# Performance work log

Measured on AMD Instinct MI355X. Metric: run time of the kernel, lower is better.

Reference implementation:

```python
import jax, jax.numpy as jnp
import numpy as np
import math


def closest_square_factors(N):
    s = int(math.isqrt(N))
    for i in range(s, 0, -1):
        if N % i == 0:
            return (i, N // i)


def landmark_pool(t, num_landmarks):
    # t: [B, H, N, Dh]; CLS token kept, rest avg-pooled on a 2D grid to num_landmarks.
    B, H, N, Dh = t.shape
    w1, w2 = closest_square_factors(N - 1)   # token grid (32, 32)
    h, w = closest_square_factors(num_landmarks)  # landmark grid (8, 8)
    assert w1 % h == 0 and w2 % w == 0  # divisible -> adaptive pool == uniform pool
    cls = t[:, :, :1, :]
    rest = t[:, :, 1:, :].reshape(B, H, h, w1 // h, w, w2 // w, Dh)
    pooled = rest.mean(axis=(3, 5)).reshape(B, H, num_landmarks, Dh)
    return jnp.concatenate([cls, pooled], axis=2)  # [B, H, num_landmarks+1, Dh]


def moore_penrose_iter_pinv(x, iters=6):
    # x: [..., m, m]; iterative Newton-Schulz style pseudo-inverse.
    abs_x = jnp.abs(x)
    col = abs_x.sum(axis=-1)
    row = abs_x.sum(axis=-2)
    z = jnp.swapaxes(x, -1, -2) / (jnp.max(col) * jnp.max(row) + 1e-15)
    I = jnp.eye(x.shape[-1], dtype=x.dtype)
    for _ in range(iters):
        xz = x @ z
        z = 0.25 * z @ (13.0 * I - xz @ (15.0 * I - xz @ (7.0 * I - xz)))
    return z


def setup_inputs() -> dict:
    key = jax.random.key(0)
    k0, k1, k2 = jax.random.split(key, 3)
    B, N, C = 32, 1025, 768
    x = jax.random.normal(k0, (B, N, C), dtype=jnp.float32)
    qkv_w = jax.random.normal(k1, (C, 3 * C), dtype=jnp.float32) * 0.02
    qkv_b = jnp.zeros((3 * C,), dtype=jnp.float32)
    proj_w = jax.random.normal(k2, (C, C), dtype=jnp.float32) * 0.02
    proj_b = jnp.zeros((C,), dtype=jnp.float32)
    return {"x": x, "qkv_w": qkv_w, "qkv_b": qkv_b, "proj_w": proj_w, "proj_b": proj_b}


def reference(x, qkv_w, qkv_b, proj_w, proj_b):
    num_heads, num_landmarks, pinv_iters = 12, 64, 6
    B, N, C = x.shape
    Dh = C // num_heads
    scale = Dh ** -0.5
    qkv = (x @ qkv_w + qkv_b).reshape(B, N, 3, num_heads, Dh).transpose(2, 0, 3, 1, 4)
    q, k, v = qkv[0] * scale, qkv[1], qkv[2]  # each [B, H, N, Dh]
    q_m = landmark_pool(q, num_landmarks)  # [B, H, m1, Dh], m1 = num_landmarks+1
    k_m = landmark_pool(k, num_landmarks)
    S_A = q @ jnp.swapaxes(k_m, -1, -2)   # [B, H, N, m1]
    S_C = q_m @ jnp.swapaxes(k, -1, -2)   # [B, H, m1, N]
    S_B = q_m @ jnp.swapaxes(k_m, -1, -2)  # [B, H, m1, m1]
    maxC = S_C.max(axis=-1, keepdims=True)
    expA = jnp.exp(S_A - S_A.max(axis=-1, keepdims=True))
    expC = jnp.exp(S_C - maxC)
    expB = jnp.exp(jnp.maximum(S_B - maxC, -88.0))
    v_aug = jnp.concatenate([v, jnp.ones_like(v[..., :1])], axis=-1)  # [B, H, N, Dh+1]
    pinv = moore_penrose_iter_pinv(expB, pinv_iters)
    prod = expA @ (pinv @ (expC @ v_aug))  # [B, H, N, Dh+1]
    ctx = prod[..., :-1] / jnp.maximum(prod[..., -1:], 1e-8)
    ctx = ctx.transpose(0, 2, 1, 3).reshape(B, N, C)
    return ctx @ proj_w + proj_b
```

## Files before the change

kernel.cpp:

```cpp
#include <hip/hip_runtime.h>
#include <hip/hip_fp16.h>


constexpr int kN  = 1025;
constexpr int kNT = 32 * kN;
constexpr int kBH = 32 * 12;
constexpr int NSPLIT = 4;

constexpr size_t QSZ  = (size_t)kBH * kN * 64;
constexpr size_t QMSZ = (size_t)kBH * 65 * 64;
constexpr size_t SBSZ = (size_t)kBH * 65 * 65;

typedef _Float16 f16x8 __attribute__((ext_vector_type(8)));
typedef float    f32x4 __attribute__((ext_vector_type(4)));

#define GLDS(gp, lp) __builtin_amdgcn_global_load_lds( \
    (const __attribute__((address_space(1))) void*)(gp), \
    (__attribute__((address_space(3))) void*)(lp), 16, 0, 0)

__device__ __forceinline__ float4 loadh4(const __half* p) {
    const __half2* q = (const __half2*)p;
    float2 a = __half22float2(q[0]);
    float2 b = __half22float2(q[1]);
    return make_float4(a.x, a.y, b.x, b.y);
}

__global__ __launch_bounds__(256) void cvt_f32_f16(
    const float* __restrict__ src, __half* __restrict__ dst, int n4)
{
    int i = blockIdx.x * 256 + threadIdx.x;
    if (i < n4) {
        float4 v = ((const float4*)src)[i];
        __half2 h01 = __floats2half2_rn(v.x, v.y);
        __half2 h23 = __floats2half2_rn(v.z, v.w);
        ((__half2*)dst)[2 * i]     = h01;
        ((__half2*)dst)[2 * i + 1] = h23;
    }
}

__global__ __launch_bounds__(256) void cvt_transpose(
    const float* __restrict__ W, __half* __restrict__ WT, int rows, int cols)
{
    __shared__ float tile[32][33];
    const int n0 = blockIdx.x * 32, k0 = blockIdx.y * 32;
#pragma unroll
    for (int i = 0; i < 4; ++i)
        tile[threadIdx.y + i * 8][threadIdx.x] =
            W[(size_t)(k0 + threadIdx.y + i * 8) * cols + n0 + threadIdx.x];
    __syncthreads();
#pragma unroll
    for (int i = 0; i < 4; ++i)
        WT[(size_t)(n0 + threadIdx.y + i * 8) * rows + k0 + threadIdx.x] =
            __float2half_rn(tile[threadIdx.x][threadIdx.y + i * 8]);
}

template<int MODE>
__global__ __launch_bounds__(256) void gemm_mfma(
    const __half* __restrict__ A, const __half* __restrict__ Bt,
    const float* __restrict__ bias,
    float* __restrict__ OutF, __half* __restrict__ Qo,
    __half* __restrict__ Ko, __half* __restrict__ Vo)
{
    __shared__ _Float16 SMEM[128 * 136];
    _Float16* As = SMEM;
    _Float16* Bs = SMEM + 128 * 64;
    const int t  = threadIdx.x;
    const int w  = t >> 6, L = t & 63;
    const int q  = L >> 4, ln = L & 15;
    const int wm = w >> 1, wn = w & 1;
    const int cb = blockIdx.x * 128, rb = blockIdx.y * 128;

    f32x4 acc[4][4];
#pragma unroll
    for (int i = 0; i < 4; ++i)
#pragma unroll
        for (int j = 0; j < 4; ++j) acc[i][j] = (f32x4)0.f;

    const int srow = L >> 3;
    const int sc   = L & 7;

    for (int kt = 0; kt < 12; ++kt) {
        const int k0 = kt * 64;
        __syncthreads();
#pragma unroll
        for (int i = 0; i < 4; ++i) {
            const int r0  = w * 32 + i * 8;
            const int row = r0 + srow;
            const int g   = sc ^ (row & 7);
            if (rb + row < kNT)
                GLDS(A + (size_t)(rb + row) * 768 + k0 + g * 8, &As[r0 * 64]);
            GLDS(Bt + (size_t)(cb + row) * 768 + k0 + g * 8, &Bs[r0 * 64]);
        }
        __syncthreads();
#pragma unroll
        for (int kc = 0; kc < 2; ++kc) {
            f16x8 af[4], bf[4];
#pragma unroll
            for (int im = 0; im < 4; ++im) {
                const int m    = wm * 64 + im * 16 + ln;
                const int slot = (kc * 4 + q) ^ (m & 7);
                af[im] = *(const f16x8*)&As[m * 64 + slot * 8];
            }
#pragma unroll
            for (int in = 0; in < 4; ++in) {
                const int n    = wn * 64 + in * 16 + ln;
                const int slot = (kc * 4 + q) ^ (n & 7);
                bf[in] = *(const f16x8*)&Bs[n * 64 + slot * 8];
            }
#pragma unroll
            for (int im = 0; im < 4; ++im)
#pragma unroll
                for (int in = 0; in < 4; ++in)
                    acc[im][in] = __builtin_amdgcn_mfma_f32_16x16x32_f16(
                        af[im], bf[in], acc[im][in], 0, 0, 0);
        }
    }

    float bcol[4];
#pragma unroll
    for (int in = 0; in < 4; ++in) bcol[in] = bias[cb + wn * 64 + in * 16 + ln];

    if (MODE == 0) {
        const int   which = cb / 768;
        const float scl   = (which == 0) ? 0.125f : 1.f;
        __syncthreads();
#pragma unroll
        for (int in = 0; in < 4; ++in) {
            const int col = wn * 64 + in * 16 + ln;
#pragma unroll
            for (int im = 0; im < 4; ++im) {
                const int rowb = wm * 64 + im * 16 + q * 4;
#pragma unroll
                for (int reg = 0; reg < 4; ++reg)
                    SMEM[(rowb + reg) * 136 + (col ^ (q << 4))] =
                        (_Float16)((acc[im][in][reg] + bcol[in]) * scl);
            }
        }
        __syncthreads();
        const int hb = (cb - which * 768) >> 6;
        __half* dstb = (which == 0) ? Qo : (which == 1) ? Ko : Vo;
#pragma unroll
        for (int s = 0; s < 8; ++s) {
            const int idx = t + s * 256;
            const int r = idx >> 4, ck = idx & 15;
            const int R = rb + r;
            if (R < kNT) {
                const int qr = (r >> 2) & 3;
                f16x8 v = *(const f16x8*)&SMEM[r * 136 + ((ck ^ (qr << 1)) << 3)];
                const int bidx = R / 1025, nn = R - bidx * 1025;
                const int h = hb + (ck >> 3), d0 = (ck & 7) * 8;
                *(f16x8*)(dstb + ((size_t)(bidx * 12 + h) * 1025 + nn) * 64 + d0) = v;
            }
        }
    } else {
#pragma unroll
        for (int im = 0; im < 4; ++im) {
            const int Rb2 = rb + wm * 64 + im * 16 + q * 4;
#pragma unroll
            for (int reg = 0; reg < 4; ++reg) {
                const int R = Rb2 + reg;
                if (R < kNT) {
#pragma unroll
                    for (int in = 0; in < 4; ++in) {
                        const int Ncol = cb + wn * 64 + in * 16 + ln;
                        OutF[(size_t)R * 768 + Ncol] = acc[im][in][reg] + bcol[in];
                    }
                }
            }
        }
    }
}

__global__ __launch_bounds__(64) void pool_kernel(
    const __half* __restrict__ Qh, const __half* __restrict__ Kh,
    float* __restrict__ QM, float* __restrict__ KM, __half* __restrict__ KMh)
{
    const int d  = threadIdx.x;
    const int m  = blockIdx.x;
    const int bh = blockIdx.y;
    if (m >= 65) {
        if (blockIdx.z == 1)
            KMh[(size_t)bh * 6144 + m * 64 + d] = __float2half_rn(0.f);
        return;
    }
    const __half* sb = (blockIdx.z ? Kh : Qh) + (size_t)bh * kN * 64;
    float* dst = blockIdx.z ? KM : QM;
    float v;
    if (m == 0) {
        v = __half2float(sb[d]);
    } else {
        int l = m - 1, a = l >> 3, e = l & 7;
        const __half* base = sb + (size_t)(1 + a * 128 + e * 4) * 64 + d;
        float s = 0.f;
#pragma unroll
        for (int b4 = 0; b4 < 4; ++b4)
#pragma unroll
            for (int f = 0; f < 4; ++f)
                s += __half2float(base[(b4 * 32 + f) * 64]);
        v = s * 0.0625f;
    }
    dst[(size_t)bh * 65 * 64 + m * 64 + d] = v;
    if (blockIdx.z == 1)
        KMh[(size_t)bh * 6144 + m * 64 + d] = __float2half_rn(v);
}

__global__ __launch_bounds__(256) void sct1_kernel(
    const float* __restrict__ QM, const __half* __restrict__ Kg,
    const __half* __restrict__ Vg, float* __restrict__ T1part,
    float* __restrict__ Mpart)
{
    __shared__ float QmT[64][68];
    __shared__ float Wt[64][68];
    __shared__ float ET[64][68];
    const int t  = threadIdx.x;
    const int sp = blockIdx.x, bh = blockIdx.y;
    const float* qm = QM + (size_t)bh * 4160;
    const __half* Kb = Kg + (size_t)bh * 65600;
    const __half* Vb = Vg + (size_t)bh * 65600;

    for (int s = 0; s < 5; ++s) {
        int idx = t + s * 256;
        if (idx < 1040) {
            int r = idx >> 4, c = idx & 15;
            float4 v = *(const float4*)(qm + r * 64 + c * 4);
            QmT[c * 4 + 0][r] = v.x; QmT[c * 4 + 1][r] = v.y;
            QmT[c * 4 + 2][r] = v.z; QmT[c * 4 + 3][r] = v.w;
        }
    }
    const int tm = t >> 4, tn = t & 15;
    float acc2[5][5];
    float run_m[5];
#pragma unroll
    for (int i = 0; i < 5; ++i) {
        run_m[i] = -1e30f;
#pragma unroll
        for (int j = 0; j < 5; ++j) acc2[i][j] = 0.f;
    }

    const int tstart = (sp == 0) ? 0 : 1 + 4 * sp;
    const int tcount = (sp == 0) ? 5 : 4;

    for (int tt = 0; tt < tcount; ++tt) {
        const int n0 = (tstart + tt) * 64;
        __syncthreads();
        for (int s = 0; s < 4; ++s) {
            int idx = t + s * 256;
            int r = idx >> 4, c = idx & 15;
            int n = n0 + r;
            float4 v = make_float4(0.f, 0.f, 0.f, 0.f);
            if (n < kN) v = loadh4(Kb + (size_t)n * 64 + c * 4);
            Wt[c * 4 + 0][r] = v.x; Wt[c * 4 + 1][r] = v.y;
            Wt[c * 4 + 2][r] = v.z; Wt[c * 4 + 3][r] = v.w;
        }
        __syncthreads();
        float acc[5][4];
#pragma unroll
        for (int i = 0; i < 5; ++i)
#pragma unroll
            for (int j = 0; j < 4; ++j) acc[i][j] = 0.f;
        for (int k = 0; k < 64; ++k) {
            float a[5], b[4];
            float4 av = *(const float4*)&QmT[k][tm * 4];
            a[0] = av.x; a[1] = av.y; a[2] = av.z; a[3] = av.w;
            a[4] = (tm == 0) ? QmT[k][64] : 0.f;
            float4 bv = *(const float4*)&Wt[k][tn * 4];
            b[0] = bv.x; b[1] = bv.y; b[2] = bv.z; b[3] = bv.w;
#pragma unroll
            for (int i = 0; i < 5; ++i)
#pragma unroll
                for (int j = 0; j < 4; ++j)
                    acc[i][j] = fmaf(a[i], b[j], acc[i][j]);
        }
        float tmax[5];
#pragma unroll
        for (int i = 0; i < 5; ++i) tmax[i] = -3e38f;
#pragma unroll
        for (int j = 0; j < 4; ++j) {
            if (n0 + tn * 4 + j < kN) {
#pragma unroll
                for (int i = 0; i < 4; ++i) tmax[i] = fmaxf(tmax[i], acc[i][j]);
                if (tm == 0) tmax[4] = fmaxf(tmax[4], acc[4][j]);
            }
        }
#pragma unroll
        for (int mk = 1; mk < 16; mk <<= 1)
#pragma unroll
            for (int i = 0; i < 5; ++i)
                tmax[i] = fmaxf(tmax[i], __shfl_xor(tmax[i], mk));
        float nm[5];
#pragma unroll
        for (int i = 0; i < 5; ++i) {
            nm[i] = fmaxf(run_m[i], tmax[i]);
            float f = __expf(run_m[i] - nm[i]);
            run_m[i] = nm[i];
#pragma unroll
            for (int j = 0; j < 5; ++j) acc2[i][j] *= f;
        }
#pragma unroll
        for (int j = 0; j < 4; ++j) {
            int nn = tn * 4 + j;
            bool valid = (n0 + nn) < kN;
#pragma unroll
            for (int i = 0; i < 4; ++i)
                ET[nn][tm * 4 + i] = valid ? __expf(acc[i][j] - nm[i]) : 0.f;
            if (tm == 0)
                ET[nn][64] = valid ? __expf(acc[4][j] - nm[4]) : 0.f;
        }
        __syncthreads();
        for (int s = 0; s < 4; ++s) {
            int idx = t + s * 256;
            int r = idx >> 4, c = idx & 15;
            int n = n0 + r;
            float4 v = make_float4(0.f, 0.f, 0.f, 0.f);
            if (n < kN) v = loadh4(Vb + (size_t)n * 64 + c * 4);
            *(float4*)&Wt[r][c * 4] = v;
        }
        if (t < 64) Wt[t][64] = 1.f;
        __syncthreads();
        for (int nn = 0; nn < 64; ++nn) {
            float a[5], b[5];
            float4 av = *(const float4*)&ET[nn][tm * 4];
            a[0] = av.x; a[1] = av.y; a[2] = av.z; a[3] = av.w;
            a[4] = (tm == 0) ? ET[nn][64] : 0.f;
            float4 bv = *(const float4*)&Wt[nn][tn * 4];
            b[0] = bv.x; b[1] = bv.y; b[2] = bv.z; b[3] = bv.w;
            b[4] = (tn == 0) ? Wt[nn][64] : 0.f;
#pragma unroll
            for (int i = 0; i < 5; ++i)
#pragma unroll
                for (int j = 0; j < 5; ++j)
                    acc2[i][j] = fmaf(a[i], b[j], acc2[i][j]);
        }
    }
    float* T1b = T1part + ((size_t)bh * NSPLIT + sp) * 4225;
#pragma unroll
    for (int i = 0; i < 5; ++i) {
        if (i == 4 && tm != 0) continue;
        int m = (i < 4) ? tm * 4 + i : 64;
#pragma unroll
        for (int j = 0; j < 5; ++j) {
            if (j == 4 && tn != 0) continue;
            int jc = (j < 4) ? tn * 4 + j : 64;
            T1b[m * 65 + jc] = acc2[i][j];
        }
    }
    if (tn == 0) {
        float* Mb = Mpart + ((size_t)bh * NSPLIT + sp) * 65;
#pragma unroll
        for (int i = 0; i < 4; ++i) Mb[tm * 4 + i] = run_m[i];
        if (tm == 0) Mb[64] = run_m[4];
    }
}

__global__ __launch_bounds__(256) void t1comb_kernel(
    const float* __restrict__ T1part, const float* __restrict__ Mpart,
    float* __restrict__ T1, float* __restrict__ MAXC)
{
    __shared__ float w[NSPLIT][65];
    const int t = threadIdx.x, bh = blockIdx.x;
    const float* Mb = Mpart + (size_t)bh * NSPLIT * 65;
    if (t < 65) {
        float m0 = Mb[t], m1 = Mb[65 + t], m2 = Mb[130 + t], m3 = Mb[195 + t];
        float M = fmaxf(fmaxf(m0, m1), fmaxf(m2, m3));
        MAXC[(size_t)bh * 65 + t] = M;
        w[0][t] = __expf(m0 - M); w[1][t] = __expf(m1 - M);
        w[2][t] = __expf(m2 - M); w[3][t] = __expf(m3 - M);
    }
    __syncthreads();
    const float* Tb = T1part + (size_t)bh * NSPLIT * 4225;
    float* To = T1 + (size_t)bh * 4225;
    for (int s = 0; s < 17; ++s) {
        int o = t + s * 256;
        if (o < 4225) {
            int m = o / 65;
            To[o] = w[0][m] * Tb[o] + w[1][m] * Tb[4225 + o]
                  + w[2][m] * Tb[8450 + o] + w[3][m] * Tb[12675 + o];
        }
    }
}

__global__ __launch_bounds__(512) void expb_kernel(
    const float* __restrict__ QM, const float* __restrict__ KM,
    const float* __restrict__ MAXC, float* __restrict__ EXPB,
    float* __restrict__ RC)
{
    __shared__ float Qs[65][68];
    __shared__ float Ks[65][68];
    __shared__ float SB[65][68];
    __shared__ float mc[65];
    __shared__ float rs[65], cs[65];
    const int t = threadIdx.x, bh = blockIdx.x;
    const float* qm = QM + (size_t)bh * 4160;
    const float* km = KM + (size_t)bh * 4160;
    for (int s = 0; s < 3; ++s) {
        int idx = t + s * 512;
        if (idx < 1040) {
            int r = idx >> 4, c = (idx & 15) * 4;
            *(float4*)&Qs[r][c] = *(const float4*)(qm + r * 64 + c);
            *(float4*)&Ks[r][c] = *(const float4*)(km + r * 64 + c);
        }
    }
    if (t < 65) mc[t] = MAXC[(size_t)bh * 65 + t];
    __syncthreads();

    const int tm = t >> 4, tj = t & 15;
    float acc[3][5];
#pragma unroll
    for (int i = 0; i < 3; ++i)
#pragma unroll
        for (int j = 0; j < 5; ++j) acc[i][j] = 0.f;
#pragma unroll 2
    for (int k4 = 0; k4 < 64; k4 += 4) {
        float Qa[3][4], Kb[5][4];
#pragma unroll
        for (int i = 0; i < 3; ++i) {
            float4 v4 = (i < 2) ? *(const float4*)&Qs[2 * tm + i][k4]
                                : *(const float4*)&Qs[64][k4];
            Qa[i][0] = v4.x; Qa[i][1] = v4.y; Qa[i][2] = v4.z; Qa[i][3] = v4.w;
        }
#pragma unroll
        for (int j = 0; j < 5; ++j) {
            float4 v4 = (j < 4) ? *(const float4*)&Ks[tj * 4 + j][k4]
                                : *(const float4*)&Ks[64][k4];
            Kb[j][0] = v4.x; Kb[j][1] = v4.y; Kb[j][2] = v4.z; Kb[j][3] = v4.w;
        }
#pragma unroll
        for (int kk = 0; kk < 4; ++kk)
#pragma unroll
            for (int i = 0; i < 3; ++i)
#pragma unroll
                for (int j = 0; j < 5; ++j)
                    acc[i][j] = fmaf(Qa[i][kk], Kb[j][kk], acc[i][j]);
    }
#pragma unroll
    for (int i = 0; i < 3; ++i) {
        if (i == 2 && tm != 0) continue;
        const int mi = (i < 2) ? 2 * tm + i : 64;
        const float mci = mc[mi];
#pragma unroll
        for (int j = 0; j < 5; ++j) {
            if (j == 4 && tj != 0) continue;
            const int jc = (j < 4) ? tj * 4 + j : 64;
            SB[mi][jc] = __expf(fmaxf(acc[i][j] - mci, -88.f));
        }
    }
    __syncthreads();
    for (int s = 0; s < 9; ++s) {
        int o = t + s * 512;
        if (o < 4225) EXPB[(size_t)bh * 4225 + o] = SB[o / 65][o % 65];
    }
    if (t < 65) {
        float r = 0.f, c = 0.f;
        for (int j = 0; j < 65; ++j) r += SB[t][j];
        for (int i = 0; i < 65; ++i) c += SB[i][t];
        rs[t] = r; cs[t] = c;
    }
    __syncthreads();
    if (t == 0) {
        float rm = 0.f, cm2 = 0.f;
        for (int i = 0; i < 65; ++i) { rm = fmaxf(rm, rs[i]); cm2 = fmaxf(cm2, cs[i]); }
        RC[bh * 2] = rm; RC[bh * 2 + 1] = cm2;
    }
}

__global__ __launch_bounds__(256) void alpha_kernel(
    const float* __restrict__ RC, float* __restrict__ GMX)
{
    __shared__ float sr[256], sc[256];
    const int t = threadIdx.x;
    float rm = 0.f, cm = 0.f;
    for (int i = t; i < kBH; i += 256) {
        rm = fmaxf(rm, RC[2 * i]);
        cm = fmaxf(cm, RC[2 * i + 1]);
    }
    sr[t] = rm; sc[t] = cm;
    __syncthreads();
    for (int s = 128; s > 0; s >>= 1) {
        if (t < s) { sr[t] = fmaxf(sr[t], sr[t + s]); sc[t] = fmaxf(sc[t], sc[t + s]); }
        __syncthreads();
    }
    if (t == 0) GMX[0] = 1.f / (sr[0] * sc[0] + 1e-15f);
}

__device__ __forceinline__ void mm65(const float (*Op1)[68], const float (*Op2)[68],
                                     float (*Dst)[68], const float (*Pre)[68],
                                     float c0, float c1, int tm, int tj)
{
    float acc[3][5];
#pragma unroll
    for (int i = 0; i < 3; ++i)
#pragma unroll
        for (int j = 0; j < 5; ++j) acc[i][j] = 0.f;
#pragma unroll 2
    for (int k4 = 0; k4 < 64; k4 += 4) {
        float Aa[3][4], Bb[4][4], c64[4];
#pragma unroll
        for (int i = 0; i < 3; ++i) {
            float4 v4 = (i < 2) ? *(const float4*)&Op1[2 * tm + i][k4]
                                : *(const float4*)&Op1[64][k4];
            Aa[i][0] = v4.x; Aa[i][1] = v4.y; Aa[i][2] = v4.z; Aa[i][3] = v4.w;
        }
#pragma unroll
        for (int kk = 0; kk < 4; ++kk) {
            float4 v4 = *(const float4*)&Op2[k4 + kk][tj * 4];
            Bb[kk][0] = v4.x; Bb[kk][1] = v4.y; Bb[kk][2] = v4.z; Bb[kk][3] = v4.w;
            c64[kk] = Op2[k4 + kk][64];
        }
#pragma unroll
        for (int kk = 0; kk < 4; ++kk)
#pragma unroll
            for (int i = 0; i < 3; ++i) {
                const float av = Aa[i][kk];
#pragma unroll
                for (int j = 0; j < 4; ++j)
                    acc[i][j] = fmaf(av, Bb[kk][j], acc[i][j]);
                acc[i][4] = fmaf(av, c64[kk], acc[i][4]);
            }
    }
    {
        float a3[3], b5[5];
        a3[0] = Op1[2 * tm][64]; a3[1] = Op1[2 * tm + 1][64]; a3[2] = Op1[64][64];
#pragma unroll
        for (int j = 0; j < 4; ++j) b5[j] = Op2[64][tj * 4 + j];
        b5[4] = Op2[64][64];
#pragma unroll
        for (int i = 0; i < 3; ++i)
#pragma unroll
            for (int j = 0; j < 5; ++j)
                acc[i][j] = fmaf(a3[i], b5[j], acc[i][j]);
    }
    float val[3][5];
#pragma unroll
    for (int i = 0; i < 3; ++i) {
        int mi = (i < 2) ? 2 * tm + i : 64;
#pragma unroll
        for (int j = 0; j < 5; ++j) {
            int jc = (j < 4) ? tj * 4 + j : 64;
            val[i][j] = c1 * (c0 * Pre[mi][jc] - acc[i][j]);
        }
    }
    __syncthreads();
#pragma unroll
    for (int i = 0; i < 3; ++i) {
        if (i == 2 && tm != 0) continue;
        int mi = (i < 2) ? 2 * tm + i : 64;
#pragma unroll
        for (int j = 0; j < 5; ++j) {
            if (j == 4 && tj != 0) continue;
            int jc = (j < 4) ? tj * 4 + j : 64;
            Dst[mi][jc] = val[i][j];
        }
    }
    __syncthreads();
}

__global__ __launch_bounds__(512) void pinv_kernel(
    const float* __restrict__ EXPB, const float* __restrict__ T1,
    const float* __restrict__ GMX, __half* __restrict__ T2TH)
{
    __shared__ float Wb[65][68];
    __shared__ float Zb[65][68];
    __shared__ float Ab[65][68];
    const int t = threadIdx.x, bh = blockIdx.x;
    const int tm = t >> 4, tj = t & 15;
    const float alpha = GMX[0];
    const float* X = EXPB + (size_t)bh * 4225;
    for (int s = 0; s < 9; ++s) {
        int o = t + s * 512;
        if (o < 4225) Wb[o / 65][o % 65] = X[o];
    }
    __syncthreads();
    for (int s = 0; s < 9; ++s) {
        int o = t + s * 512;
        if (o < 4225) { int i = o / 65, j = o % 65; Zb[i][j] = alpha * Wb[j][i]; }
    }
    __syncthreads();
    for (int it = 0; it < 6; ++it) {
        if (it > 0) {
            for (int s = 0; s < 9; ++s) {
                int o = t + s * 512;
                if (o < 4225) Wb[o / 65][o % 65] = X[o];
            }
            __syncthreads();
        }
        mm65(Wb, Zb, Ab, Wb, 0.f,  -1.f,  tm, tj);
        mm65(Ab, Ab, Wb, Ab, 7.f,   1.f,  tm, tj);
        mm65(Ab, Wb, Ab, Ab, 15.f,  1.f,  tm, tj);
        mm65(Zb, Ab, Zb, Zb, 13.f,  0.25f, tm, tj);
    }
    for (int s = 0; s < 9; ++s) {
        int o = t + s * 512;
        if (o < 4225) Wb[o / 65][o % 65] = T1[(size_t)bh * 4225 + o];
    }
    __syncthreads();
    {
        float acc[3][5];
#pragma unroll
        for (int i = 0; i < 3; ++i)
#pragma unroll
            for (int j = 0; j < 5; ++j) acc[i][j] = 0.f;
#pragma unroll 2
        for (int k4 = 0; k4 < 64; k4 += 4) {
            float Aa[3][4], Bb[4][4], c64[4];
#pragma unroll
            for (int i = 0; i < 3; ++i) {
                float4 v4 = (i < 2) ? *(const float4*)&Zb[2 * tm + i][k4]
                                    : *(const float4*)&Zb[64][k4];
                Aa[i][0] = v4.x; Aa[i][1] = v4.y; Aa[i][2] = v4.z; Aa[i][3] = v4.w;
            }
#pragma unroll
            for (int kk = 0; kk < 4; ++kk) {
                float4 v4 = *(const float4*)&Wb[k4 + kk][tj * 4];
                Bb[kk][0] = v4.x; Bb[kk][1] = v4.y; Bb[kk][2] = v4.z; Bb[kk][3] = v4.w;
                c64[kk] = Wb[k4 + kk][64];
            }
#pragma unroll
            for (int kk = 0; kk < 4; ++kk)
#pragma unroll
                for (int i = 0; i < 3; ++i) {
                    const float av = Aa[i][kk];
#pragma unroll
                    for (int j = 0; j < 4; ++j)
                        acc[i][j] = fmaf(av, Bb[kk][j], acc[i][j]);
                    acc[i][4] = fmaf(av, c64[kk], acc[i][4]);
                }
        }
        {
            float a3[3], b5[5];
            a3[0] = Zb[2 * tm][64]; a3[1] = Zb[2 * tm + 1][64]; a3[2] = Zb[64][64];
#pragma unroll
            for (int j = 0; j < 4; ++j) b5[j] = Wb[64][tj * 4 + j];
            b5[4] = Wb[64][64];
#pragma unroll
            for (int i = 0; i < 3; ++i)
#pragma unroll
                for (int j = 0; j < 5; ++j)
                    acc[i][j] = fmaf(a3[i], b5[j], acc[i][j]);
        }
        __syncthreads();
#pragma unroll
        for (int i = 0; i < 3; ++i) {
            if (i == 2 && tm != 0) continue;
            int mi = (i < 2) ? 2 * tm + i : 64;
#pragma unroll
            for (int j = 0; j < 5; ++j) {
                if (j == 4 && tj != 0) continue;
                int jc = (j < 4) ? tj * 4 + j : 64;
                Ab[mi][jc] = acc[i][j];
            }
        }
    }
    __syncthreads();
    __half* dstT = T2TH + (size_t)bh * 7680;
    for (int o = t; o < 7680; o += 512) {
        int n = o / 96, k = o - n * 96;
        float v = (n < 65 && k < 65) ? Ab[k][n] : 0.f;
        dstT[o] = __float2half_rn(v);
    }
}

__global__ __launch_bounds__(256) void prod_mfma(
    const __half* __restrict__ Qg, const __half* __restrict__ KMh,
    const __half* __restrict__ T2TH, __half* __restrict__ CTXh)
{
    __shared__ _Float16 Ps[128 * 104];
    __shared__ float dn[128];
    const int t = threadIdx.x;
    const int w = t >> 6, L = t & 63;
    const int q = L >> 4, ln = L & 15;
    const int nb = blockIdx.x, bh = blockIdx.y;
    const int bq = bh / 12, h = bh % 12;
    const int n0 = nb * 128;
    const __half* Qb  = Qg   + (size_t)bh * 65600;
    const __half* Kmb = KMh  + (size_t)bh * 6144;
    const __half* Tb  = T2TH + (size_t)bh * 7680;

    f32x4 accA[2][6];
#pragma unroll
    for (int i = 0; i < 2; ++i)
#pragma unroll
        for (int j = 0; j < 6; ++j) accA[i][j] = (f32x4)0.f;

#pragma unroll
    for (int kc = 0; kc < 2; ++kc) {
        f16x8 af[2], bf[6];
#pragma unroll
        for (int im = 0; im < 2; ++im) {
            int r = n0 + w * 32 + im * 16 + ln;
            if (r > 1024) r = 1024;
            af[im] = *(const f16x8*)(Qb + (size_t)r * 64 + (kc * 4 + q) * 8);
        }
#pragma unroll
        for (int in = 0; in < 6; ++in)
            bf[in] = *(const f16x8*)(Kmb + (size_t)(in * 16 + ln) * 64 + (kc * 4 + q) * 8);
#pragma unroll
        for (int im = 0; im < 2; ++im)
#pragma unroll
            for (int in = 0; in < 6; ++in)
                accA[im][in] = __builtin_amdgcn_mfma_f32_16x16x32_f16(
                    af[im], bf[in], accA[im][in], 0, 0, 0);
    }
#pragma unroll
    for (int im = 0; im < 2; ++im) {
        const int row = w * 32 + im * 16 + q * 4;
#pragma unroll
        for (int in = 0; in < 6; ++in) {
            const int col = in * 16 + ln;
#pragma unroll
            for (int reg = 0; reg < 4; ++reg)
                Ps[(row + reg) * 104 + col] = (_Float16)__expf(accA[im][in][reg]);
        }
    }
    __syncthreads();

    f32x4 accB[2][5];
#pragma unroll
    for (int i = 0; i < 2; ++i)
#pragma unroll
        for (int j = 0; j < 5; ++j) accB[i][j] = (f32x4)0.f;
#pragma unroll
    for (int kc = 0; kc < 3; ++kc) {
        f16x8 pa[2], tb[5];
#pragma unroll
        for (int im = 0; im < 2; ++im)
            pa[im] = *(const f16x8*)&Ps[(w * 32 + im * 16 + ln) * 104 + (kc * 4 + q) * 8];
#pragma unroll
        for (int in = 0; in < 5; ++in)
            tb[in] = *(const f16x8*)(Tb + (size_t)(in * 16 + ln) * 96 + (kc * 4 + q) * 8);
#pragma unroll
        for (int im = 0; im < 2; ++im)
#pragma unroll
            for (int in = 0; in < 5; ++in)
                accB[im][in] = __builtin_amdgcn_mfma_f32_16x16x32_f16(
                    pa[im], tb[in], accB[im][in], 0, 0, 0);
    }
    if (ln == 0) {
#pragma unroll
        for (int im = 0; im < 2; ++im) {
            const int row = w * 32 + im * 16 + q * 4;
#pragma unroll
            for (int reg = 0; reg < 4; ++reg)
                dn[row + reg] = accB[im][4][reg];
        }
    }
    __syncthreads();
#pragma unroll
    for (int im = 0; im < 2; ++im) {
        const int rowb = w * 32 + im * 16 + q * 4;
#pragma unroll
        for (int reg = 0; reg < 4; ++reg) {
            const int n = n0 + rowb + reg;
            if (n < kN) {
                const float dv = fmaxf(dn[rowb + reg], 1e-8f);
                __half* dst = CTXh + ((size_t)bq * 1025 + n) * 768 + h * 64;
#pragma unroll
                for (int in = 0; in < 4; ++in)
                    dst[in * 16 + ln] = __float2half_rn(accB[im][in][reg] / dv);
            }
        }
    }
}

extern "C" void kernel_launch(void* const* d_in, const int* in_sizes, int n_in,
                              void* d_out, int out_size, void* d_ws, size_t ws_size,
                              hipStream_t stream)
{
    const float* x      = (const float*)d_in[0];
    const float* qkv_w  = (const float*)d_in[1];
    const float* qkv_b  = (const float*)d_in[2];
    const float* proj_w = (const float*)d_in[3];
    const float* proj_b = (const float*)d_in[4];
    float* out = (float*)d_out;

    __half* Xh = (__half*)d_out;
    __half* Qh = Xh + QSZ;
    float*  T1part = (float*)d_out;
    float*  Mpart  = T1part + (size_t)kBH * NSPLIT * 4225;
    __half* KMh  = (__half*)((char*)d_out + (size_t)27 * 1024 * 1024);
    __half* T2TH = (__half*)((char*)d_out + (size_t)33 * 1024 * 1024);

    __half* Kh   = (__half*)d_ws;
    __half* Vh   = Kh + QSZ;
    __half* CTXh = Kh;
    float*  QM   = (float*)(Vh + QSZ);
    float*  KM   = QM + QMSZ;
    float*  MAXC = KM + QMSZ;
    float*  EXPB = MAXC + (size_t)kBH * 65;
    float*  T1   = EXPB + SBSZ;
    float*  T2   = T1 + SBSZ;
    float*  RC   = T2 + SBSZ;
    float*  GMX  = RC + (size_t)kBH * 2;
    size_t woff = (size_t)(GMX + 1 - (float*)d_ws);
    woff = (woff + 3) & ~(size_t)3;
    __half* WqkvT = (__half*)((float*)d_ws + woff);
    __half* WprojT = WqkvT + (size_t)2304 * 768;

    cvt_f32_f16  <<<dim3((int)(QSZ / 4 / 256)), 256, 0, stream>>>(x, Xh, (int)(QSZ / 4));
    cvt_transpose<<<dim3(72, 24), dim3(32, 8), 0, stream>>>(qkv_w, WqkvT, 768, 2304);
    cvt_transpose<<<dim3(24, 24), dim3(32, 8), 0, stream>>>(proj_w, WprojT, 768, 768);

    gemm_mfma<0><<<dim3(18, 257), 256, 0, stream>>>(Xh, WqkvT, qkv_b,
                                                    nullptr, Qh, Kh, Vh);
    pool_kernel<<<dim3(96, kBH, 2), 64, 0, stream>>>(Qh, Kh, QM, KM, KMh);
    sct1_kernel<<<dim3(NSPLIT, kBH), 256, 0, stream>>>(QM, Kh, Vh, T1part, Mpart);
    t1comb_kernel<<<dim3(kBH), 256, 0, stream>>>(T1part, Mpart, T1, MAXC);
    expb_kernel<<<dim3(kBH), 512, 0, stream>>>(QM, KM, MAXC, EXPB, RC);
    alpha_kernel<<<dim3(1), 256, 0, stream>>>(RC, GMX);
    pinv_kernel<<<dim3(kBH), 512, 0, stream>>>(EXPB, T1, GMX, T2TH);
    prod_mfma  <<<dim3(9, kBH), 256, 0, stream>>>(Qh, KMh, T2TH, CTXh);
    gemm_mfma<1><<<dim3(6, 257), 256, 0, stream>>>(CTXh, WprojT, proj_b,
                                                   out, nullptr, nullptr, nullptr);
}
```

Before: 872.7 us.

## Move expC@V_aug stage to MFMA with a separate row-max pass

```diff
diff --git a/kernel.cpp b/kernel.cpp
--- a/kernel.cpp
+++ b/kernel.cpp
@@ -173,7 +173,8 @@
 
 __global__ __launch_bounds__(64) void pool_kernel(
     const __half* __restrict__ Qh, const __half* __restrict__ Kh,
-    float* __restrict__ QM, float* __restrict__ KM, __half* __restrict__ KMh)
+    float* __restrict__ QM, float* __restrict__ KM,
+    __half* __restrict__ KMh, __half* __restrict__ QMh)
 {
     const int d  = threadIdx.x;
     const int m  = blockIdx.x;
@@ -181,6 +182,8 @@
     if (m >= 65) {
         if (blockIdx.z == 1)
             KMh[(size_t)bh * 6144 + m * 64 + d] = __float2half_rn(0.f);
+        else if (m < 80)
+            QMh[(size_t)bh * 5120 + m * 64 + d] = __float2half_rn(0.f);
         return;
     }
     const __half* sb = (blockIdx.z ? Kh : Qh) + (size_t)bh * kN * 64;
@@ -202,186 +205,210 @@
     dst[(size_t)bh * 65 * 64 + m * 64 + d] = v;
     if (blockIdx.z == 1)
         KMh[(size_t)bh * 6144 + m * 64 + d] = __float2half_rn(v);
-}
-
-__global__ __launch_bounds__(256) void sct1_kernel(
-    const float* __restrict__ QM, const __half* __restrict__ Kg,
-    const __half* __restrict__ Vg, float* __restrict__ T1part,
-    float* __restrict__ Mpart)
-{
-    __shared__ float QmT[64][68];
-    __shared__ float Wt[64][68];
-    __shared__ float ET[64][68];
-    const int t  = threadIdx.x;
+    else
+        QMh[(size_t)bh * 5120 + m * 64 + d] = __float2half_rn(v);
+}
+
+__global__ __launch_bounds__(256) void maxc_mfma(
+    const __half* __restrict__ QMh, const __half* __restrict__ Kg,
+    float* __restrict__ MAXCp)
+{
+    __shared__ _Float16 QmS[80 * 72];
+    __shared__ float mxW[4][80];
+    const int t = threadIdx.x;
+    const int w = t >> 6, L = t & 63;
+    const int q = L >> 4, ln = L & 15;
     const int sp = blockIdx.x, bh = blockIdx.y;
-    const float* qm = QM + (size_t)bh * 4160;
-    const __half* Kb = Kg + (size_t)bh * 65600;
-    const __half* Vb = Vg + (size_t)bh * 65600;
-
-    for (int s = 0; s < 5; ++s) {
+    const __half* Kb  = Kg  + (size_t)bh * 65600;
+    const __half* Qmb = QMh + (size_t)bh * 5120;
+
+    for (int s = 0; s < 3; ++s) {
         int idx = t + s * 256;
-        if (idx < 1040) {
-            int r = idx >> 4, c = idx & 15;
-            float4 v = *(const float4*)(qm + r * 64 + c * 4);
-            QmT[c * 4 + 0][r] = v.x; QmT[c * 4 + 1][r] = v.y;
-            QmT[c * 4 + 2][r] = v.z; QmT[c * 4 + 3][r] = v.w;
-        }
-    }
-    const int tm = t >> 4, tn = t & 15;
-    float acc2[5][5];
-    float run_m[5];
-#pragma unroll
-    for (int i = 0; i < 5; ++i) {
-        run_m[i] = -1e30f;
-#pragma unroll
-        for (int j = 0; j < 5; ++j) acc2[i][j] = 0.f;
-    }
-
-    const int tstart = (sp == 0) ? 0 : 1 + 4 * sp;
-    const int tcount = (sp == 0) ? 5 : 4;
-
-    for (int tt = 0; tt < tcount; ++tt) {
-        const int n0 = (tstart + tt) * 64;
+        if (idx < 640) {
+            int r = idx >> 3, c8 = idx & 7;
+            *(f16x8*)&QmS[r * 72 + c8 * 8] = *(const f16x8*)(Qmb + r * 64 + c8 * 8);
+        }
+    }
+    const int ns = sp * 256;
+    const int ne = (sp == 3) ? 1025 : ns + 256;
+    f32x4 run[5];
+#pragma unroll
+    for (int im = 0; im < 5; ++im) run[im] = (f32x4)(-3e38f);
+    __syncthreads();
+    const int nch = (ne - ns + 63) >> 6;
+    for (int c = 0; c < nch; ++c) {
+        const int nc = ns + c * 64;
+        const int n = nc + w * 16 + ln;
+        const int n_eff = (n > 1024) ? 1024 : n;
+        f32x4 accA[5];
+#pragma unroll
+        for (int im = 0; im < 5; ++im) accA[im] = (f32x4)0.f;
+#pragma unroll
+        for (int kc = 0; kc < 2; ++kc) {
+            f16x8 bf = *(const f16x8*)(Kb + (size_t)n_eff * 64 + (kc * 4 + q) * 8);
+#pragma unroll
+            for (int im = 0; im < 5; ++im) {
+                f16x8 af = *(const f16x8*)&QmS[(im * 16 + ln) * 72 + (kc * 4 + q) * 8];
+                accA[im] = __builtin_amdgcn_mfma_f32_16x16x32_f16(af, bf, accA[im], 0, 0, 0);
+            }
+        }
+        const bool valid = n < ne;
+#pragma unroll
+        for (int im = 0; im < 5; ++im)
+#pragma unroll
+            for (int reg = 0; reg < 4; ++reg)
+                run[im][reg] = fmaxf(run[im][reg], valid ? accA[im][reg] : -3e38f);
+    }
+#pragma unroll
+    for (int mk = 1; mk < 16; mk <<= 1)
+#pragma unroll
+        for (int im = 0; im < 5; ++im)
+#pragma unroll
+            for (int reg = 0; reg < 4; ++reg)
+                run[im][reg] = fmaxf(run[im][reg], __shfl_xor(run[im][reg], mk));
+    if (ln == 0) {
+#pragma unroll
+        for (int im = 0; im < 5; ++im)
+#pragma unroll
+            for (int reg = 0; reg < 4; ++reg)
+                mxW[w][im * 16 + q * 4 + reg] = run[im][reg];
+    }
+    __syncthreads();
+    if (t < 65)
+        MAXCp[((size_t)bh * NSPLIT + sp) * 80 + t] =
+            fmaxf(fmaxf(mxW[0][t], mxW[1][t]), fmaxf(mxW[2][t], mxW[3][t]));
+}
+
+__global__ __launch_bounds__(256) void sct1_mfma(
+    const __half* __restrict__ QMh, const __half* __restrict__ Kg,
+    const __half* __restrict__ Vg, const float* __restrict__ MAXCp,
+    float* __restrict__ T1part)
+{
+    __shared__ _Float16 QmS[80 * 72];
+    __shared__ _Float16 ExpS[80 * 72];
+    __shared__ _Float16 VT[80 * 72];
+    __shared__ float mcS[80];
+    const int t = threadIdx.x;
+    const int w = t >> 6, L = t & 63;
+    const int q = L >> 4, ln = L & 15;
+    const int sp = blockIdx.x, bh = blockIdx.y;
+    const __half* Kb  = Kg  + (size_t)bh * 65600;
+    const __half* Vb  = Vg  + (size_t)bh * 65600;
+    const __half* Qmb = QMh + (size_t)bh * 5120;
+
+    for (int s = 0; s < 3; ++s) {
+        int idx = t + s * 256;
+        if (idx < 640) {
+            int r = idx >> 3, c8 = idx & 7;
+            *(f16x8*)&QmS[r * 72 + c8 * 8] = *(const f16x8*)(Qmb + r * 64 + c8 * 8);
+        }
+    }
+    if (t < 80) {
+        float m = 0.f;
+        if (t < 65) {
+            const float* P = MAXCp + (size_t)bh * NSPLIT * 80;
+            m = fmaxf(fmaxf(P[t], P[80 + t]), fmaxf(P[160 + t], P[240 + t]));
+        }
+        mcS[t] = m;
+    }
+    const int ns = sp * 256;
+    const int ne = (sp == 3) ? 1025 : ns + 256;
+
+    f32x4 acc2[2][5];
+#pragma unroll
+    for (int i = 0; i < 2; ++i)
+#pragma unroll
+        for (int j = 0; j < 5; ++j) acc2[i][j] = (f32x4)0.f;
+    __syncthreads();
+
+    const int nch = (ne - ns + 63) >> 6;
+    for (int c = 0; c < nch; ++c) {
+        const int nc = ns + c * 64;
+        {
+            const int nl = t >> 2, d0 = (t & 3) * 16;
+            const int n = nc + nl;
+            const int n_eff = (n > 1024) ? 1024 : n;
+            f16x8 v0 = *(const f16x8*)(Vb + (size_t)n_eff * 64 + d0);
+            f16x8 v1 = *(const f16x8*)(Vb + (size_t)n_eff * 64 + d0 + 8);
+#pragma unroll
+            for (int j = 0; j < 8; ++j) VT[(d0 + j) * 72 + nl] = v0[j];
+#pragma unroll
+            for (int j = 0; j < 8; ++j) VT[(d0 + 8 + j) * 72 + nl] = v1[j];
+        }
+        if (t < 64) {
+            VT[64 * 72 + t] = (_Float16)1.f;
+#pragma unroll
+            for (int r = 65; r < 80; ++r) VT[r * 72 + t] = (_Float16)0.f;
+        }
+        f32x4 accA[5];
+#pragma unroll
+        for (int im = 0; im < 5; ++im) accA[im] = (f32x4)0.f;
+        {
+            const int n = nc + w * 16 + ln;
+            const int n_eff = (n > 1024) ? 1024 : n;
+#pragma unroll
+            for (int kc = 0; kc < 2; ++kc) {
+                f16x8 bf = *(const f16x8*)(Kb + (size_t)n_eff * 64 + (kc * 4 + q) * 8);
+#pragma unroll
+                for (int im = 0; im < 5; ++im) {
+                    f16x8 af = *(const f16x8*)&QmS[(im * 16 + ln) * 72 + (kc * 4 + q) * 8];
+                    accA[im] = __builtin_amdgcn_mfma_f32_16x16x32_f16(
+                        af, bf, accA[im], 0, 0, 0);
+                }
+            }
+        }
+        {
+            const bool valid = (nc + w * 16 + ln) < ne;
+            const int colL = w * 16 + ln;
+#pragma unroll
+            for (int im = 0; im < 5; ++im) {
+                const int rowb = im * 16 + q * 4;
+#pragma unroll
+                for (int reg = 0; reg < 4; ++reg)
+                    ExpS[(rowb + reg) * 72 + colL] =
+                        valid ? (_Float16)__expf(accA[im][reg] - mcS[rowb + reg])
+                              : (_Float16)0.f;
+            }
+        }
         __syncthreads();
-        for (int s = 0; s < 4; ++s) {
-            int idx = t + s * 256;
-            int r = idx >> 4, c = idx & 15;
-            int n = n0 + r;
-            float4 v = make_float4(0.f, 0.f, 0.f, 0.f);
-            if (n < kN) v = loadh4(Kb + (size_t)n * 64 + c * 4);
-            Wt[c * 4 + 0][r] = v.x; Wt[c * 4 + 1][r] = v.y;
-            Wt[c * 4 + 2][r] = v.z; Wt[c * 4 + 3][r] = v.w;
+#pragma unroll
+        for (int tt = 0; tt < 2; ++tt) {
+            if (tt == 1 && w != 0) break;
+            const int mt = (tt == 0) ? w : 4;
+#pragma unroll
+            for (int kc = 0; kc < 2; ++kc) {
+                f16x8 pa = *(const f16x8*)&ExpS[(mt * 16 + ln) * 72 + (kc * 4 + q) * 8];
+#pragma unroll
+                for (int jn = 0; jn < 5; ++jn) {
+                    f16x8 vb = *(const f16x8*)&VT[(jn * 16 + ln) * 72 + (kc * 4 + q) * 8];
+                    acc2[tt][jn] = __builtin_amdgcn_mfma_f32_16x16x32_f16(
+                        pa, vb, acc2[tt][jn], 0, 0, 0);
+                }
+            }
         }
         __syncthreads();
-        float acc[5][4];
-#pragma unroll
-        for (int i = 0; i < 5; ++i)
-#pragma unroll
-            for (int j = 0; j < 4; ++j) acc[i][j] = 0.f;
-        for (int k = 0; k < 64; ++k) {
-            float a[5], b[4];
-            float4 av = *(const float4*)&QmT[k][tm * 4];
-            a[0] = av.x; a[1] = av.y; a[2] = av.z; a[3] = av.w;
-            a[4] = (tm == 0) ? QmT[k][64] : 0.f;
-            float4 bv = *(const float4*)&Wt[k][tn * 4];
-            b[0] = bv.x; b[1] = bv.y; b[2] = bv.z; b[3] = bv.w;
-#pragma unroll
-            for (int i = 0; i < 5; ++i)
-#pragma unroll
-                for (int j = 0; j < 4; ++j)
-                    acc[i][j] = fmaf(a[i], b[j], acc[i][j]);
-        }
-        float tmax[5];
-#pragma unroll
-        for (int i = 0; i < 5; ++i) tmax[i] = -3e38f;
-#pragma unroll
-        for (int j = 0; j < 4; ++j) {
-            if (n0 + tn * 4 + j < kN) {
-#pragma unroll
-                for (int i = 0; i < 4; ++i) tmax[i] = fmaxf(tmax[i], acc[i][j]);
-                if (tm == 0) tmax[4] = fmaxf(tmax[4], acc[4][j]);
-            }
-        }
-#pragma unroll
-        for (int mk = 1; mk < 16; mk <<= 1)
-#pragma unroll
-            for (int i = 0; i < 5; ++i)
-                tmax[i] = fmaxf(tmax[i], __shfl_xor(tmax[i], mk));
-        float nm[5];
-#pragma unroll
-        for (int i = 0; i < 5; ++i) {
-            nm[i] = fmaxf(run_m[i], tmax[i]);
-            float f = __expf(run_m[i] - nm[i]);
-            run_m[i] = nm[i];
-#pragma unroll
-            for (int j = 0; j < 5; ++j) acc2[i][j] *= f;
-        }
-#pragma unroll
-        for (int j = 0; j < 4; ++j) {
-            int nn = tn * 4 + j;
-            bool valid = (n0 + nn) < kN;
-#pragma unroll
-            for (int i = 0; i < 4; ++i)
-                ET[nn][tm * 4 + i] = valid ? __expf(acc[i][j] - nm[i]) : 0.f;
-            if (tm == 0)
-                ET[nn][64] = valid ? __expf(acc[4][j] - nm[4]) : 0.f;
-        }
-        __syncthreads();
-        for (int s = 0; s < 4; ++s) {
-            int idx = t + s * 256;
-            int r = idx >> 4, c = idx & 15;
-            int n = n0 + r;
-            float4 v = make_float4(0.f, 0.f, 0.f, 0.f);
-            if (n < kN) v = loadh4(Vb + (size_t)n * 64 + c * 4);
-            *(float4*)&Wt[r][c * 4] = v;
-        }
-        if (t < 64) Wt[t][64] = 1.f;
-        __syncthreads();
-        for (int nn = 0; nn < 64; ++nn) {
-            float a[5], b[5];
-            float4 av = *(const float4*)&ET[nn][tm * 4];
-            a[0] = av.x; a[1] = av.y; a[2] = av.z; a[3] = av.w;
-            a[4] = (tm == 0) ? ET[nn][64] : 0.f;
-            float4 bv = *(const float4*)&Wt[nn][tn * 4];
-            b[0] = bv.x; b[1] = bv.y; b[2] = bv.z; b[3] = bv.w;
-            b[4] = (tn == 0) ? Wt[nn][64] : 0.f;
-#pragma unroll
-            for (int i = 0; i < 5; ++i)
-#pragma unroll
-                for (int j = 0; j < 5; ++j)
-                    acc2[i][j] = fmaf(a[i], b[j], acc2[i][j]);
-        }
     }
     float* T1b = T1part + ((size_t)bh * NSPLIT + sp) * 4225;
 #pragma unroll
-    for (int i = 0; i < 5; ++i) {
-        if (i == 4 && tm != 0) continue;
-        int m = (i < 4) ? tm * 4 + i : 64;
-#pragma unroll
-        for (int j = 0; j < 5; ++j) {
-            if (j == 4 && tn != 0) continue;
-            int jc = (j < 4) ? tn * 4 + j : 64;
-            T1b[m * 65 + jc] = acc2[i][j];
-        }
-    }
-    if (tn == 0) {
-        float* Mb = Mpart + ((size_t)bh * NSPLIT + sp) * 65;
-#pragma unroll
-        for (int i = 0; i < 4; ++i) Mb[tm * 4 + i] = run_m[i];
-        if (tm == 0) Mb[64] = run_m[4];
-    }
-}
-
-__global__ __launch_bounds__(256) void t1comb_kernel(
-    const float* __restrict__ T1part, const float* __restrict__ Mpart,
-    float* __restrict__ T1, float* __restrict__ MAXC)
-{
-    __shared__ float w[NSPLIT][65];
-    const int t = threadIdx.x, bh = blockIdx.x;
-    const float* Mb = Mpart + (size_t)bh * NSPLIT * 65;
-    if (t < 65) {
-        float m0 = Mb[t], m1 = Mb[65 + t], m2 = Mb[130 + t], m3 = Mb[195 + t];
-        float M = fmaxf(fmaxf(m0, m1), fmaxf(m2, m3));
-        MAXC[(size_t)bh * 65 + t] = M;
-        w[0][t] = __expf(m0 - M); w[1][t] = __expf(m1 - M);
-        w[2][t] = __expf(m2 - M); w[3][t] = __expf(m3 - M);
-    }
-    __syncthreads();
-    const float* Tb = T1part + (size_t)bh * NSPLIT * 4225;
-    float* To = T1 + (size_t)bh * 4225;
-    for (int s = 0; s < 17; ++s) {
-        int o = t + s * 256;
-        if (o < 4225) {
-            int m = o / 65;
-            To[o] = w[0][m] * Tb[o] + w[1][m] * Tb[4225 + o]
-                  + w[2][m] * Tb[8450 + o] + w[3][m] * Tb[12675 + o];
+    for (int tt = 0; tt < 2; ++tt) {
+        if (tt == 1 && w != 0) continue;
+        const int mt = (tt == 0) ? w : 4;
+#pragma unroll
+        for (int jn = 0; jn < 5; ++jn) {
+            const int col = jn * 16 + ln;
+            if (col >= 65) continue;
+#pragma unroll
+            for (int reg = 0; reg < 4; ++reg) {
+                const int row = mt * 16 + q * 4 + reg;
+                if (row < 65) T1b[row * 65 + col] = acc2[tt][jn][reg];
+            }
         }
     }
 }
 
 __global__ __launch_bounds__(512) void expb_kernel(
     const float* __restrict__ QM, const float* __restrict__ KM,
-    const float* __restrict__ MAXC, float* __restrict__ EXPB,
+    const float* __restrict__ MAXCp, float* __restrict__ EXPB,
     float* __restrict__ RC)
 {
     __shared__ float Qs[65][68];
@@ -400,7 +427,10 @@
             *(float4*)&Ks[r][c] = *(const float4*)(km + r * 64 + c);
         }
     }
-    if (t < 65) mc[t] = MAXC[(size_t)bh * 65 + t];
+    if (t < 65) {
+        const float* P = MAXCp + (size_t)bh * NSPLIT * 80;
+        mc[t] = fmaxf(fmaxf(P[t], P[80 + t]), fmaxf(P[160 + t], P[240 + t]));
+    }
     __syncthreads();
 
     const int tm = t >> 4, tj = t & 15;
@@ -555,7 +585,7 @@
 }
 
 __global__ __launch_bounds__(512) void pinv_kernel(
-    const float* __restrict__ EXPB, const float* __restrict__ T1,
+    const float* __restrict__ EXPB, const float* __restrict__ T1part,
     const float* __restrict__ GMX, __half* __restrict__ T2TH)
 {
     __shared__ float Wb[65][68];
@@ -588,9 +618,13 @@
         mm65(Ab, Wb, Ab, Ab, 15.f,  1.f,  tm, tj);
         mm65(Zb, Ab, Zb, Zb, 13.f,  0.25f, tm, tj);
     }
-    for (int s = 0; s < 9; ++s) {
-        int o = t + s * 512;
-        if (o < 4225) Wb[o / 65][o % 65] = T1[(size_t)bh * 4225 + o];
+    {
+        const float* Tp = T1part + (size_t)bh * NSPLIT * 4225;
+        for (int s = 0; s < 9; ++s) {
+            int o = t + s * 512;
+            if (o < 4225)
+                Wb[o / 65][o % 65] = Tp[o] + Tp[4225 + o] + Tp[8450 + o] + Tp[12675 + o];
+        }
     }
     __syncthreads();
     {
@@ -775,9 +809,10 @@
     __half* Xh = (__half*)d_out;
     __half* Qh = Xh + QSZ;
     float*  T1part = (float*)d_out;
-    float*  Mpart  = T1part + (size_t)kBH * NSPLIT * 4225;
-    __half* KMh  = (__half*)((char*)d_out + (size_t)27 * 1024 * 1024);
-    __half* T2TH = (__half*)((char*)d_out + (size_t)33 * 1024 * 1024);
+    __half* KMh   = (__half*)((char*)d_out + (size_t)27 * 1024 * 1024);
+    __half* T2TH  = (__half*)((char*)d_out + (size_t)33 * 1024 * 1024);
+    __half* QMh   = (__half*)((char*)d_out + (size_t)39 * 1024 * 1024);
+    float*  MAXCp = (float*)((char*)d_out + (size_t)45 * 1024 * 1024);
 
     __half* Kh   = (__half*)d_ws;
     __half* Vh   = Kh + QSZ;
@@ -801,12 +836,12 @@
 
     gemm_mfma<0><<<dim3(18, 257), 256, 0, stream>>>(Xh, WqkvT, qkv_b,
                                                     nullptr, Qh, Kh, Vh);
-    pool_kernel<<<dim3(96, kBH, 2), 64, 0, stream>>>(Qh, Kh, QM, KM, KMh);
-    sct1_kernel<<<dim3(NSPLIT, kBH), 256, 0, stream>>>(QM, Kh, Vh, T1part, Mpart);
-    t1comb_kernel<<<dim3(kBH), 256, 0, stream>>>(T1part, Mpart, T1, MAXC);
-    expb_kernel<<<dim3(kBH), 512, 0, stream>>>(QM, KM, MAXC, EXPB, RC);
+    pool_kernel<<<dim3(96, kBH, 2), 64, 0, stream>>>(Qh, Kh, QM, KM, KMh, QMh);
+    maxc_mfma  <<<dim3(NSPLIT, kBH), 256, 0, stream>>>(QMh, Kh, MAXCp);
+    sct1_mfma  <<<dim3(NSPLIT, kBH), 256, 0, stream>>>(QMh, Kh, Vh, MAXCp, T1part);
+    expb_kernel<<<dim3(kBH), 512, 0, stream>>>(QM, KM, MAXCp, EXPB, RC);
     alpha_kernel<<<dim3(1), 256, 0, stream>>>(RC, GMX);
-    pinv_kernel<<<dim3(kBH), 512, 0, stream>>>(EXPB, T1, GMX, T2TH);
+    pinv_kernel<<<dim3(kBH), 512, 0, stream>>>(EXPB, T1part, GMX, T2TH);
     prod_mfma  <<<dim3(9, kBH), 256, 0, stream>>>(Qh, KMh, T2TH, CTXh);
     gemm_mfma<1><<<dim3(6, 257), 256, 0, stream>>>(CTXh, WprojT, proj_b,
                                                    out, nullptr, nullptr, nullptr);
```

New measurement: 733.4 us. 16.0% less time.
